# Kernel tuning notes

Hardware: AMD Instinct MI355X
Metric: run time of the kernel (lower is better)

## Reference

```python
import jax, jax.numpy as jnp
import numpy as np

B, S, D, H, P = 4, 2048, 1024, 16, 10
DK = D // H

def setup_inputs() -> dict:
    key = jax.random.key(0)
    ks = jax.random.split(key, 12)
    inp = {
        'q': jax.random.normal(ks[0], (B, S, D), jnp.float32),
        'k': jax.random.normal(ks[1], (B, S, D), jnp.float32),
        'v': jax.random.normal(ks[2], (B, S, D), jnp.float32),
        # causal mask, broadcastable over batch/heads
        'mask': jnp.tril(jnp.ones((S, S), jnp.int32))[None, None, :, :],
        'Wq': jax.random.normal(ks[3], (D, D), jnp.float32) * (1.0 / np.sqrt(D)),
        'bq': jnp.zeros((D,), jnp.float32),
        'Wk': jax.random.normal(ks[4], (D, D), jnp.float32) * (1.0 / np.sqrt(D)),
        'bk': jnp.zeros((D,), jnp.float32),
        'Wv': jax.random.normal(ks[5], (D, D), jnp.float32) * (1.0 / np.sqrt(D)),
        'bv': jnp.zeros((D,), jnp.float32),
        'Wo': jax.random.normal(ks[6], (D, D), jnp.float32) * (1.0 / np.sqrt(D)),
        'bo': jnp.zeros((D,), jnp.float32),
        'prefix_k': jax.random.normal(ks[7], (H, P, DK), jnp.float32) * 0.02,
        'prefix_v': jax.random.normal(ks[8], (H, P, DK), jnp.float32) * 0.02,
    }
    return inp

def reference(q, k, v, mask, Wq, bq, Wk, bk, Wv, bv, Wo, bo, prefix_k, prefix_v):
    bs, sq, d = q.shape
    h, p, dk = prefix_k.shape
    # projections -> [B, H, S, dk]
    Q = (q @ Wq + bq).reshape(bs, sq, h, dk).transpose(0, 2, 1, 3)
    K = (k @ Wk + bk).reshape(bs, -1, h, dk).transpose(0, 2, 1, 3)
    V = (v @ Wv + bv).reshape(bs, -1, h, dk).transpose(0, 2, 1, 3)
    # prepend learnable prefix K/V along the key axis
    pK = jnp.broadcast_to(prefix_k[None], (bs, h, p, dk))
    pV = jnp.broadcast_to(prefix_v[None], (bs, h, p, dk))
    K = jnp.concatenate([pK, K], axis=2)  # [B,H,P+S,dk]
    V = jnp.concatenate([pV, V], axis=2)
    # extend mask: prefix positions always visible
    pref_mask = jnp.ones(mask.shape[:3] + (p,), mask.dtype)
    full_mask = jnp.concatenate([pref_mask, mask], axis=-1)  # [.,.,S,P+S]
    scores = jnp.einsum('bhqd,bhkd->bhqk', Q, K) / np.sqrt(dk).astype(jnp.float32)
    scores = jnp.where(full_mask == 0, jnp.asarray(-1e9, scores.dtype), scores)
    attn = jax.nn.softmax(scores, axis=-1)  # dropout in eval mode: identity
    out = jnp.einsum('bhqk,bhkd->bhqd', attn, V)
    out = out.transpose(0, 2, 1, 3).reshape(bs, sq, d)
    return out @ Wo + bo
```

## Files before the change

### kernel.cpp

```cpp
#include <hip/hip_runtime.h>

typedef __bf16 bf16x8 __attribute__((ext_vector_type(8)));
typedef __bf16 bf16x4 __attribute__((ext_vector_type(4)));
typedef float f32x4 __attribute__((ext_vector_type(4)));

constexpr int Sq = 2048, Dd = 1024, Hn = 16, Pn = 10, DK = 64;
constexpr int SKPAD = 2112;
constexpr int NBH = 64;
constexpr float LOG2E = 1.44269504088896340736f;

__device__ __forceinline__ float exp2_fast(float x) {
  return __builtin_amdgcn_exp2f(x);
}

__device__ __forceinline__ unsigned short f2bf(float f) {
  unsigned int u = __float_as_uint(f);
  u += 0x7fffu + ((u >> 16) & 1u);
  return (unsigned short)(u >> 16);
}

__device__ __forceinline__ void gload_lds16(const void* g, void* l) {
  __builtin_amdgcn_global_load_lds(
      (const __attribute__((address_space(1))) void*)g,
      (__attribute__((address_space(3))) void*)l, 16, 0, 0);
}

__device__ __forceinline__ f32x4 mfma16(bf16x8 a, bf16x8 b, f32x4 c) {
  return __builtin_amdgcn_mfma_f32_16x16x32_bf16(a, b, c, 0, 0, 0);
}

__global__ void k_cvt3(const float* __restrict__ i0, const float* __restrict__ i1,
                       const float* __restrict__ i2, unsigned short* __restrict__ o0,
                       unsigned short* __restrict__ o1, unsigned short* __restrict__ o2,
                       int n4) {
  const float* in; unsigned short* out;
  switch (blockIdx.y) {
    case 0: in = i0; out = o0; break;
    case 1: in = i1; out = o1; break;
    default: in = i2; out = o2; break;
  }
  int i = blockIdx.x * blockDim.x + threadIdx.x;
  int st = gridDim.x * blockDim.x;
  for (; i < n4; i += st) {
    float4 v = reinterpret_cast<const float4*>(in)[i];
    ushort4 r;
    r.x = f2bf(v.x); r.y = f2bf(v.y); r.z = f2bf(v.z); r.w = f2bf(v.w);
    reinterpret_cast<ushort4*>(out)[i] = r;
  }
}

__global__ void k_wt(const float* __restrict__ W0, const float* __restrict__ W1,
                     const float* __restrict__ W2, const float* __restrict__ W3,
                     unsigned short* __restrict__ T0, unsigned short* __restrict__ T1,
                     unsigned short* __restrict__ T2, unsigned short* __restrict__ T3) {
  __shared__ float tile[32][33];
  const float* W; unsigned short* T;
  switch (blockIdx.z) {
    case 0: W = W0; T = T0; break;
    case 1: W = W1; T = T1; break;
    case 2: W = W2; T = T2; break;
    default: W = W3; T = T3; break;
  }
  int n0 = blockIdx.x * 32, k0 = blockIdx.y * 32;
  int tx = threadIdx.x, ty = threadIdx.y;
  for (int r = ty; r < 32; r += 8)
    tile[r][tx] = W[(size_t)(k0 + r) * Dd + n0 + tx];
  __syncthreads();
  for (int r = ty; r < 32; r += 8)
    T[(size_t)(n0 + r) * Dd + k0 + tx] = f2bf(tile[tx][r]);
}

__global__ void k_fill(const float* __restrict__ pk, const float* __restrict__ pv,
                       unsigned short* __restrict__ Kb, unsigned short* __restrict__ Vt) {
  int bh = blockIdx.x;
  int h = bh & (Hn - 1);
  unsigned short* Kbh = Kb + (size_t)bh * SKPAD * DK;
  unsigned short* Vth = Vt + (size_t)bh * DK * SKPAD;
  for (int i = threadIdx.x; i < Pn * DK; i += blockDim.x) {
    int p = i >> 6, dk = i & 63;
    float kv = pk[((size_t)h * Pn + p) * DK + dk];
    float vv = pv[((size_t)h * Pn + p) * DK + dk];
    Kbh[p * DK + dk] = f2bf(kv);
    Vth[dk * SKPAD + p] = f2bf(vv);
  }
  constexpr int ZR = SKPAD - (Pn + Sq);
  for (int i = threadIdx.x; i < ZR * DK; i += blockDim.x) {
    int r = i >> 6, c = i & 63;
    Kbh[(Pn + Sq + r) * DK + c] = 0;
    Vth[c * SKPAD + (Pn + Sq + r)] = 0;
  }
}

__device__ __forceinline__ void gemm_body(
    const unsigned short* __restrict__ A, const unsigned short* __restrict__ Bt,
    const float* __restrict__ bias, unsigned short* __restrict__ outB,
    float* __restrict__ outF, int mode, float scale,
    unsigned short* As, unsigned short* Bs) {
  int tid = threadIdx.x;
  int w = tid >> 6, l = tid & 63;
  int lq = l & 15, lg = l >> 4;
  int bx = blockIdx.x;
  int tm = bx >> 3, tn = bx & 7;
  int brow = tm * 128, bcol = tn * 128;
  int wm = w >> 1, wn = w & 1;

  f32x4 acc[4][4];
#pragma unroll
  for (int m = 0; m < 4; ++m)
#pragma unroll
    for (int n = 0; n < 4; ++n) acc[m][n] = (f32x4){0.f, 0.f, 0.f, 0.f};

  for (int kt = 0; kt < 1024; kt += 64) {
#pragma unroll
    for (int it = 0; it < 4; ++it) {
      int c = it * 256 + tid;
      int row = c >> 3, col = c & 7;
      gload_lds16(A + (size_t)(brow + row) * 1024 + kt + col * 8,
                  As + (size_t)(it * 256 + w * 64) * 8);
      gload_lds16(Bt + (size_t)(bcol + row) * 1024 + kt + col * 8,
                  Bs + (size_t)(it * 256 + w * 64) * 8);
    }
    asm volatile("s_waitcnt vmcnt(0)" ::: "memory");
    __syncthreads();
    const bf16x8* As8 = reinterpret_cast<const bf16x8*>(As);
    const bf16x8* Bs8 = reinterpret_cast<const bf16x8*>(Bs);
#pragma unroll
    for (int ks = 0; ks < 2; ++ks) {
      bf16x8 af[4], bfv[4];
#pragma unroll
      for (int m = 0; m < 4; ++m)
        af[m] = As8[(size_t)(wm * 64 + m * 16 + lq) * 8 + ks * 4 + lg];
#pragma unroll
      for (int n = 0; n < 4; ++n)
        bfv[n] = Bs8[(size_t)(wn * 64 + n * 16 + lq) * 8 + ks * 4 + lg];
#pragma unroll
      for (int m = 0; m < 4; ++m)
#pragma unroll
        for (int n = 0; n < 4; ++n)
          acc[m][n] = mfma16(af[m], bfv[n], acc[m][n]);
    }
    __syncthreads();
  }

#pragma unroll
  for (int n = 0; n < 4; ++n) {
    int N = bcol + wn * 64 + n * 16 + lq;
    float bv = bias[N];
#pragma unroll
    for (int m = 0; m < 4; ++m) {
      int M0 = brow + wm * 64 + m * 16 + lg * 4;
#pragma unroll
      for (int r = 0; r < 4; ++r) {
        float val = (acc[m][n][r] + bv) * scale;
        int Mr = M0 + r;
        if (mode == 3) {
          outF[(size_t)Mr * 1024 + N] = val;
        } else {
          int b = Mr >> 11, s = Mr & 2047;
          int h = N >> 6, dk = N & 63;
          size_t idx;
          if (mode == 0)      idx = (((size_t)(b * Hn + h)) * Sq + s) * DK + dk;
          else if (mode == 1) idx = (((size_t)(b * Hn + h)) * SKPAD + Pn + s) * DK + dk;
          else                idx = (((size_t)(b * Hn + h)) * DK + dk) * SKPAD + Pn + s;
          outB[idx] = f2bf(val);
        }
      }
    }
  }
}

__global__ __launch_bounds__(256, 4) void k_gemm_qkv(
    const unsigned short* __restrict__ Aq, const unsigned short* __restrict__ Ak,
    const unsigned short* __restrict__ Av,
    const unsigned short* __restrict__ Wq, const unsigned short* __restrict__ Wk,
    const unsigned short* __restrict__ Wv,
    const float* __restrict__ bq, const float* __restrict__ bk,
    const float* __restrict__ bv,
    unsigned short* __restrict__ Qo, unsigned short* __restrict__ Ko,
    unsigned short* __restrict__ Vo, float qscale) {
  __shared__ unsigned short As[128 * 64];
  __shared__ unsigned short Bs[128 * 64];
  const unsigned short *A, *Bt; const float* bias; unsigned short* outB;
  int mode; float scale;
  switch (blockIdx.y) {
    case 0:  A = Aq; Bt = Wq; bias = bq; outB = Qo; mode = 0; scale = qscale; break;
    case 1:  A = Ak; Bt = Wk; bias = bk; outB = Ko; mode = 1; scale = 1.f; break;
    default: A = Av; Bt = Wv; bias = bv; outB = Vo; mode = 2; scale = 1.f; break;
  }
  gemm_body(A, Bt, bias, outB, nullptr, mode, scale, As, Bs);
}

__global__ __launch_bounds__(256, 4) void k_gemm_o(
    const unsigned short* __restrict__ A, const unsigned short* __restrict__ Bt,
    const float* __restrict__ bias, float* __restrict__ outF) {
  __shared__ unsigned short As[128 * 64];
  __shared__ unsigned short Bs[128 * 64];
  gemm_body(A, Bt, bias, nullptr, outF, 3, 1.0f, As, Bs);
}

__global__ __launch_bounds__(256, 4) void k_attn(
    const unsigned short* __restrict__ Qb, const unsigned short* __restrict__ Kb,
    const unsigned short* __restrict__ Vt, unsigned short* __restrict__ O) {
  __shared__ unsigned short Ks[2][64 * 64];
  __shared__ unsigned short Vs[2][64 * 64];
  __shared__ unsigned short Ps[4][16 * 64];
  int tid = threadIdx.x;
  int w = tid >> 6, l = tid & 63;
  int lq = l & 15, lg = l >> 4;
  int bh = blockIdx.x;
  int pi = blockIdx.y;
  int qtL = pi, qtH = 31 - pi;
  int nktL = qtL + 2;
  int nktH = qtH + 2;
  int qsA[2] = {qtL * 64, qtH * 64};

  bf16x8 qf[2][2];
#pragma unroll
  for (int qt = 0; qt < 2; ++qt) {
    const unsigned short* Qg = Qb + ((size_t)bh * Sq + qsA[qt] + w * 16) * DK;
#pragma unroll
    for (int ks = 0; ks < 2; ++ks)
      qf[qt][ks] = *reinterpret_cast<const bf16x8*>(
          Qg + (size_t)lq * DK + ks * 32 + lg * 8);
  }

  const unsigned short* Kg = Kb + (size_t)bh * SKPAD * DK;
  const unsigned short* Vg = Vt + (size_t)bh * DK * SKPAD;

  float m_run[2] = {-1e30f, -1e30f};
  float l_part[2] = {0.f, 0.f};
  f32x4 oacc[2][4];
#pragma unroll
  for (int qt = 0; qt < 2; ++qt)
#pragma unroll
    for (int n = 0; n < 4; ++n) oacc[qt][n] = (f32x4){0.f, 0.f, 0.f, 0.f};

  unsigned short* Pw = &Ps[w][0];

  auto STAGE = [&](int b, int t) {
    int kt = t * 64;
#pragma unroll
    for (int it = 0; it < 2; ++it) {
      int dst = (it * 256 + tid) * 16;
      int srcK = dst ^ (((dst >> 7) & 7) << 4);
      gload_lds16((const char*)(Kg + (size_t)kt * DK) + srcK,
                  (char*)Ks[b] + (size_t)(it * 256 + w * 64) * 16);
    }
#pragma unroll
    for (int it = 0; it < 2; ++it) {
      int dst = (it * 256 + tid) * 16;
      int row = dst >> 7;
      int colb = (dst & 127) ^ ((row & 7) << 4);
      gload_lds16((const char*)(Vg + (size_t)row * SKPAD + kt) + colb,
                  (char*)Vs[b] + (size_t)(it * 256 + w * 64) * 16);
    }
  };

  STAGE(0, 0);
  asm volatile("s_waitcnt vmcnt(0)" ::: "memory");
  __syncthreads();

  for (int t = 0; t < nktH; ++t) {
    int bsel = t & 1;
    if (t + 1 < nktH) STAGE(bsel ^ 1, t + 1);
    int kt = t * 64;

#pragma unroll
    for (int qt = 0; qt < 2; ++qt) {
      if (qt == 0 && t >= nktL) continue;
      int qs = qsA[qt];
      if (kt > qs + w * 16 + 15 + Pn) continue;

      f32x4 st[4];
#pragma unroll
      for (int m = 0; m < 4; ++m) st[m] = (f32x4){0.f, 0.f, 0.f, 0.f};
      __builtin_amdgcn_s_setprio(1);
#pragma unroll
      for (int ks = 0; ks < 2; ++ks) {
#pragma unroll
        for (int m = 0; m < 4; ++m) {
          int krow = m * 16 + lq;
          int byt = (krow * 128 + ks * 64 + lg * 16) ^ ((krow & 7) << 4);
          bf16x8 kf = *reinterpret_cast<const bf16x8*>((const char*)Ks[bsel] + byt);
          st[m] = mfma16(kf, qf[qt][ks], st[m]);
        }
      }
      __builtin_amdgcn_s_setprio(0);

      if (kt + 63 > qs + w * 16 + Pn) {
        int qrowP = qs + w * 16 + lq + Pn;
#pragma unroll
        for (int m = 0; m < 4; ++m)
#pragma unroll
          for (int r = 0; r < 4; ++r) {
            int key = kt + m * 16 + lg * 4 + r;
            st[m][r] = (key <= qrowP) ? st[m][r] : -1e30f;
          }
      }

      float mx = fmaxf(fmaxf(st[0][0], st[0][1]), fmaxf(st[0][2], st[0][3]));
#pragma unroll
      for (int m = 1; m < 4; ++m)
        mx = fmaxf(mx, fmaxf(fmaxf(st[m][0], st[m][1]), fmaxf(st[m][2], st[m][3])));
      if (__any(mx > m_run[qt] + 8.f)) {
        float gmx = fmaxf(mx, __shfl_xor(mx, 16));
        gmx = fmaxf(gmx, __shfl_xor(gmx, 32));
        float mnew = fmaxf(m_run[qt], gmx);
        float alpha = exp2_fast(m_run[qt] - mnew);
        m_run[qt] = mnew;
        l_part[qt] *= alpha;
        float ar[4];
#pragma unroll
        for (int r = 0; r < 4; ++r) ar[r] = __shfl(alpha, lg * 4 + r);
#pragma unroll
        for (int n = 0; n < 4; ++n)
#pragma unroll
          for (int r = 0; r < 4; ++r) oacc[qt][n][r] *= ar[r];
      }
      float rs = 0.f;
#pragma unroll
      for (int m = 0; m < 4; ++m) {
        bf16x4 p4;
#pragma unroll
        for (int r = 0; r < 4; ++r) {
          float p = exp2_fast(st[m][r] - m_run[qt]);
          rs += p;
          p4[r] = (__bf16)p;
        }
        int byt = (lq * 128 + m * 32 + lg * 8) ^ ((lq & 7) << 4);
        *reinterpret_cast<bf16x4*>((char*)Pw + byt) = p4;
      }
      l_part[qt] += rs;

      __builtin_amdgcn_s_setprio(1);
#pragma unroll
      for (int ks = 0; ks < 2; ++ks) {
        int pbyt = (lq * 128 + ks * 64 + lg * 16) ^ ((lq & 7) << 4);
        bf16x8 pf = *reinterpret_cast<const bf16x8*>((const char*)Pw + pbyt);
#pragma unroll
        for (int n = 0; n < 4; ++n) {
          int dv = n * 16 + lq;
          int vbyt = (dv * 128 + ks * 64 + lg * 16) ^ ((dv & 7) << 4);
          bf16x8 vf = *reinterpret_cast<const bf16x8*>((const char*)Vs[bsel] + vbyt);
          oacc[qt][n] = mfma16(pf, vf, oacc[qt][n]);
        }
      }
      __builtin_amdgcn_s_setprio(0);
    }
    asm volatile("s_waitcnt vmcnt(0)" ::: "memory");
    __syncthreads();
  }

  int b = bh >> 4, h = bh & 15;
#pragma unroll
  for (int qt = 0; qt < 2; ++qt) {
    float ls = l_part[qt];
    ls += __shfl_xor(ls, 16);
    ls += __shfl_xor(ls, 32);
    float lr[4];
#pragma unroll
    for (int r = 0; r < 4; ++r) lr[r] = 1.0f / __shfl(ls, lg * 4 + r);
#pragma unroll
    for (int n = 0; n < 4; ++n)
#pragma unroll
      for (int r = 0; r < 4; ++r) {
        int qrow2 = qsA[qt] + w * 16 + lg * 4 + r;
        size_t idx = ((size_t)b * Sq + qrow2) * Dd + h * DK + n * 16 + lq;
        O[idx] = f2bf(oacc[qt][n][r] * lr[r]);
      }
  }
}

extern "C" void kernel_launch(void* const* d_in, const int* in_sizes, int n_in,
                              void* d_out, int out_size, void* d_ws, size_t ws_size,
                              hipStream_t stream) {
  (void)in_sizes; (void)n_in; (void)out_size; (void)ws_size;
  const float* q  = (const float*)d_in[0];
  const float* k  = (const float*)d_in[1];
  const float* v  = (const float*)d_in[2];
  const float* Wq = (const float*)d_in[4];
  const float* bq = (const float*)d_in[5];
  const float* Wk = (const float*)d_in[6];
  const float* bk = (const float*)d_in[7];
  const float* Wv = (const float*)d_in[8];
  const float* bv = (const float*)d_in[9];
  const float* Wo = (const float*)d_in[10];
  const float* bo = (const float*)d_in[11];
  const float* pk = (const float*)d_in[12];
  const float* pv = (const float*)d_in[13];

  unsigned short* wsp = (unsigned short*)d_ws;
  size_t off = 0;
  auto take = [&](size_t elems) { unsigned short* p = wsp + off; off += elems; return p; };
  unsigned short* qc  = take(8388608);
  unsigned short* kc  = take(8388608);
  unsigned short* vc  = take(8388608);
  unsigned short* wqt = take(1048576);
  unsigned short* wkt = take(1048576);
  unsigned short* wvt = take(1048576);
  unsigned short* wot = take(1048576);
  unsigned short* Qbf = take(8388608);
  unsigned short* KbB = take((size_t)NBH * SKPAD * DK);
  unsigned short* VtB = take((size_t)NBH * DK * SKPAD);
  unsigned short* Ob  = qc;
  float* outF = (float*)d_out;

  k_cvt3<<<dim3(1024, 3), 256, 0, stream>>>(q, k, v, qc, kc, vc, 8388608 / 4);
  k_wt<<<dim3(32, 32, 4), dim3(32, 8), 0, stream>>>(Wq, Wk, Wv, Wo, wqt, wkt, wvt, wot);
  k_fill<<<64, 256, 0, stream>>>(pk, pv, KbB, VtB);
  k_gemm_qkv<<<dim3(512, 3), 256, 0, stream>>>(qc, kc, vc, wqt, wkt, wvt,
                                               bq, bk, bv, Qbf, KbB, VtB,
                                               0.125f * LOG2E);
  k_attn<<<dim3(NBH, 16), 256, 0, stream>>>(Qbf, KbB, VtB, Ob);
  k_gemm_o<<<512, 256, 0, stream>>>(Ob, wot, bo, outF);
}
```

Before: 222.5 us.

## Fuse fp32-to-bf16 input conversion into QKV GEMM and remap block order

Removes the separate k_cvt3 kernel that converted q/k/v to bf16. The QKV GEMM now reads fp32 activations directly, converts them in registers and writes bf16 tiles to LDS, so the intermediate bf16 arrays are never written and re-read. Both GEMMs also get a flat 1D grid with a remapped block index, which changes which tiles run together and may improve L2 reuse of weights. The cost is that each activation tile is reloaded and reconverted once per N-tile (8 times), and the A loads become synchronous register loads instead of async global-to-LDS copies.

```diff
diff --git a/kernel.cpp b/kernel.cpp
--- a/kernel.cpp
+++ b/kernel.cpp
@@ -27,26 +27,6 @@
 
 __device__ __forceinline__ f32x4 mfma16(bf16x8 a, bf16x8 b, f32x4 c) {
   return __builtin_amdgcn_mfma_f32_16x16x32_bf16(a, b, c, 0, 0, 0);
-}
-
-__global__ void k_cvt3(const float* __restrict__ i0, const float* __restrict__ i1,
-                       const float* __restrict__ i2, unsigned short* __restrict__ o0,
-                       unsigned short* __restrict__ o1, unsigned short* __restrict__ o2,
-                       int n4) {
-  const float* in; unsigned short* out;
-  switch (blockIdx.y) {
-    case 0: in = i0; out = o0; break;
-    case 1: in = i1; out = o1; break;
-    default: in = i2; out = o2; break;
-  }
-  int i = blockIdx.x * blockDim.x + threadIdx.x;
-  int st = gridDim.x * blockDim.x;
-  for (; i < n4; i += st) {
-    float4 v = reinterpret_cast<const float4*>(in)[i];
-    ushort4 r;
-    r.x = f2bf(v.x); r.y = f2bf(v.y); r.z = f2bf(v.z); r.w = f2bf(v.w);
-    reinterpret_cast<ushort4*>(out)[i] = r;
-  }
 }
 
 __global__ void k_wt(const float* __restrict__ W0, const float* __restrict__ W1,
@@ -91,87 +71,9 @@
   }
 }
 
-__device__ __forceinline__ void gemm_body(
-    const unsigned short* __restrict__ A, const unsigned short* __restrict__ Bt,
-    const float* __restrict__ bias, unsigned short* __restrict__ outB,
-    float* __restrict__ outF, int mode, float scale,
-    unsigned short* As, unsigned short* Bs) {
-  int tid = threadIdx.x;
-  int w = tid >> 6, l = tid & 63;
-  int lq = l & 15, lg = l >> 4;
-  int bx = blockIdx.x;
-  int tm = bx >> 3, tn = bx & 7;
-  int brow = tm * 128, bcol = tn * 128;
-  int wm = w >> 1, wn = w & 1;
-
-  f32x4 acc[4][4];
-#pragma unroll
-  for (int m = 0; m < 4; ++m)
-#pragma unroll
-    for (int n = 0; n < 4; ++n) acc[m][n] = (f32x4){0.f, 0.f, 0.f, 0.f};
-
-  for (int kt = 0; kt < 1024; kt += 64) {
-#pragma unroll
-    for (int it = 0; it < 4; ++it) {
-      int c = it * 256 + tid;
-      int row = c >> 3, col = c & 7;
-      gload_lds16(A + (size_t)(brow + row) * 1024 + kt + col * 8,
-                  As + (size_t)(it * 256 + w * 64) * 8);
-      gload_lds16(Bt + (size_t)(bcol + row) * 1024 + kt + col * 8,
-                  Bs + (size_t)(it * 256 + w * 64) * 8);
-    }
-    asm volatile("s_waitcnt vmcnt(0)" ::: "memory");
-    __syncthreads();
-    const bf16x8* As8 = reinterpret_cast<const bf16x8*>(As);
-    const bf16x8* Bs8 = reinterpret_cast<const bf16x8*>(Bs);
-#pragma unroll
-    for (int ks = 0; ks < 2; ++ks) {
-      bf16x8 af[4], bfv[4];
-#pragma unroll
-      for (int m = 0; m < 4; ++m)
-        af[m] = As8[(size_t)(wm * 64 + m * 16 + lq) * 8 + ks * 4 + lg];
-#pragma unroll
-      for (int n = 0; n < 4; ++n)
-        bfv[n] = Bs8[(size_t)(wn * 64 + n * 16 + lq) * 8 + ks * 4 + lg];
-#pragma unroll
-      for (int m = 0; m < 4; ++m)
-#pragma unroll
-        for (int n = 0; n < 4; ++n)
-          acc[m][n] = mfma16(af[m], bfv[n], acc[m][n]);
-    }
-    __syncthreads();
-  }
-
-#pragma unroll
-  for (int n = 0; n < 4; ++n) {
-    int N = bcol + wn * 64 + n * 16 + lq;
-    float bv = bias[N];
-#pragma unroll
-    for (int m = 0; m < 4; ++m) {
-      int M0 = brow + wm * 64 + m * 16 + lg * 4;
-#pragma unroll
-      for (int r = 0; r < 4; ++r) {
-        float val = (acc[m][n][r] + bv) * scale;
-        int Mr = M0 + r;
-        if (mode == 3) {
-          outF[(size_t)Mr * 1024 + N] = val;
-        } else {
-          int b = Mr >> 11, s = Mr & 2047;
-          int h = N >> 6, dk = N & 63;
-          size_t idx;
-          if (mode == 0)      idx = (((size_t)(b * Hn + h)) * Sq + s) * DK + dk;
-          else if (mode == 1) idx = (((size_t)(b * Hn + h)) * SKPAD + Pn + s) * DK + dk;
-          else                idx = (((size_t)(b * Hn + h)) * DK + dk) * SKPAD + Pn + s;
-          outB[idx] = f2bf(val);
-        }
-      }
-    }
-  }
-}
-
 __global__ __launch_bounds__(256, 4) void k_gemm_qkv(
-    const unsigned short* __restrict__ Aq, const unsigned short* __restrict__ Ak,
-    const unsigned short* __restrict__ Av,
+    const float* __restrict__ Aq, const float* __restrict__ Ak,
+    const float* __restrict__ Av,
     const unsigned short* __restrict__ Wq, const unsigned short* __restrict__ Wk,
     const unsigned short* __restrict__ Wv,
     const float* __restrict__ bq, const float* __restrict__ bk,
@@ -180,14 +82,101 @@
     unsigned short* __restrict__ Vo, float qscale) {
   __shared__ unsigned short As[128 * 64];
   __shared__ unsigned short Bs[128 * 64];
-  const unsigned short *A, *Bt; const float* bias; unsigned short* outB;
-  int mode; float scale;
-  switch (blockIdx.y) {
-    case 0:  A = Aq; Bt = Wq; bias = bq; outB = Qo; mode = 0; scale = qscale; break;
-    case 1:  A = Ak; Bt = Wk; bias = bk; outB = Ko; mode = 1; scale = 1.f; break;
-    default: A = Av; Bt = Wv; bias = bv; outB = Vo; mode = 2; scale = 1.f; break;
-  }
-  gemm_body(A, Bt, bias, outB, nullptr, mode, scale, As, Bs);
+  int bx0 = blockIdx.x;
+  int orig = (bx0 & 7) * 192 + (bx0 >> 3);
+  int stream = orig >> 9, within = orig & 511;
+
+  const float* A32; const unsigned short* Bt; const float* bias;
+  unsigned short* outB; float scale;
+  switch (stream) {
+    case 0:  A32 = Aq; Bt = Wq; bias = bq; outB = Qo; scale = qscale; break;
+    case 1:  A32 = Ak; Bt = Wk; bias = bk; outB = Ko; scale = 1.f; break;
+    default: A32 = Av; Bt = Wv; bias = bv; outB = Vo; scale = 1.f; break;
+  }
+
+  int tid = threadIdx.x;
+  int w = tid >> 6, l = tid & 63;
+  int lq = l & 15, lg = l >> 4;
+  int tm = within >> 3, tn = within & 7;
+  int brow = tm * 128, bcol = tn * 128;
+  int wm = w >> 1, wn = w & 1;
+
+  f32x4 acc[4][4];
+#pragma unroll
+  for (int m = 0; m < 4; ++m)
+#pragma unroll
+    for (int n = 0; n < 4; ++n) acc[m][n] = (f32x4){0.f, 0.f, 0.f, 0.f};
+
+  int arow = tid >> 3, acol = tid & 7;
+
+  for (int kt = 0; kt < 1024; kt += 64) {
+#pragma unroll
+    for (int it = 0; it < 4; ++it) {
+      int c = it * 256 + tid;
+      int row = c >> 3, col = c & 7;
+      gload_lds16(Bt + (size_t)(bcol + row) * 1024 + kt + col * 8,
+                  Bs + (size_t)(it * 256 + w * 64) * 8);
+    }
+    float4 a0[4], a1[4];
+#pragma unroll
+    for (int it = 0; it < 4; ++it) {
+      const float* src = A32 + (size_t)(brow + it * 32 + arow) * 1024 + kt + acol * 8;
+      a0[it] = *reinterpret_cast<const float4*>(src);
+      a1[it] = *reinterpret_cast<const float4*>(src + 4);
+    }
+#pragma unroll
+    for (int it = 0; it < 4; ++it) {
+      ushort4 lo, hi;
+      lo.x = f2bf(a0[it].x); lo.y = f2bf(a0[it].y);
+      lo.z = f2bf(a0[it].z); lo.w = f2bf(a0[it].w);
+      hi.x = f2bf(a1[it].x); hi.y = f2bf(a1[it].y);
+      hi.z = f2bf(a1[it].z); hi.w = f2bf(a1[it].w);
+      ushort4* dst = reinterpret_cast<ushort4*>(As + (size_t)(it * 256 + tid) * 8);
+      dst[0] = lo; dst[1] = hi;
+    }
+    asm volatile("s_waitcnt vmcnt(0)" ::: "memory");
+    __syncthreads();
+    const bf16x8* As8 = reinterpret_cast<const bf16x8*>(As);
+    const bf16x8* Bs8 = reinterpret_cast<const bf16x8*>(Bs);
+#pragma unroll
+    for (int ks = 0; ks < 2; ++ks) {
+      bf16x8 af[4], bfv[4];
+#pragma unroll
+      for (int m = 0; m < 4; ++m)
+        af[m] = As8[(size_t)(wm * 64 + m * 16 + lq) * 8 + ks * 4 + lg];
+#pragma unroll
+      for (int n = 0; n < 4; ++n)
+        bfv[n] = Bs8[(size_t)(wn * 64 + n * 16 + lq) * 8 + ks * 4 + lg];
+#pragma unroll
+      for (int m = 0; m < 4; ++m)
+#pragma unroll
+        for (int n = 0; n < 4; ++n)
+          acc[m][n] = mfma16(af[m], bfv[n], acc[m][n]);
+    }
+    __syncthreads();
+  }
+
+#pragma unroll
+  for (int n = 0; n < 4; ++n) {
+    int N = bcol + wn * 64 + n * 16 + lq;
+    float bv = bias[N];
+#pragma unroll
+    for (int m = 0; m < 4; ++m) {
+      int M0 = brow + wm * 64 + m * 16 + lg * 4;
+#pragma unroll
+      for (int r = 0; r < 4; ++r) {
+        float val = (acc[m][n][r] + bv) * scale;
+        int Mr = M0 + r;
+        int b = Mr >> 11, s = Mr & 2047;
+        int h = N >> 6, dk = N & 63;
+        size_t idx;
+        if (stream == 0)      idx = (((size_t)(b * Hn + h)) * Sq + s) * DK + dk;
+        else if (stream == 1) idx = (((size_t)(b * Hn + h)) * SKPAD + Pn + s) * DK + dk;
+        else                  idx = (((size_t)(b * Hn + h)) * DK + dk) * SKPAD + Pn + s;
+        outB[idx] = f2bf(val);
+      }
+    }
+  }
 }
 
 __global__ __launch_bounds__(256, 4) void k_gemm_o(
@@ -195,7 +184,65 @@
     const float* __restrict__ bias, float* __restrict__ outF) {
   __shared__ unsigned short As[128 * 64];
   __shared__ unsigned short Bs[128 * 64];
-  gemm_body(A, Bt, bias, nullptr, outF, 3, 1.0f, As, Bs);
+  int bx0 = blockIdx.x;
+  int within = (bx0 & 7) * 64 + (bx0 >> 3);
+  int tid = threadIdx.x;
+  int w = tid >> 6, l = tid & 63;
+  int lq = l & 15, lg = l >> 4;
+  int tm = within >> 3, tn = within & 7;
+  int brow = tm * 128, bcol = tn * 128;
+  int wm = w >> 1, wn = w & 1;
+
+  f32x4 acc[4][4];
+#pragma unroll
+  for (int m = 0; m < 4; ++m)
+#pragma unroll
+    for (int n = 0; n < 4; ++n) acc[m][n] = (f32x4){0.f, 0.f, 0.f, 0.f};
+
+  for (int kt = 0; kt < 1024; kt += 64) {
+#pragma unroll
+    for (int it = 0; it < 4; ++it) {
+      int c = it * 256 + tid;
+      int row = c >> 3, col = c & 7;
+      gload_lds16(A + (size_t)(brow + row) * 1024 + kt + col * 8,
+                  As + (size_t)(it * 256 + w * 64) * 8);
+      gload_lds16(Bt + (size_t)(bcol + row) * 1024 + kt + col * 8,
+                  Bs + (size_t)(it * 256 + w * 64) * 8);
+    }
+    asm volatile("s_waitcnt vmcnt(0)" ::: "memory");
+    __syncthreads();
+    const bf16x8* As8 = reinterpret_cast<const bf16x8*>(As);
+    const bf16x8* Bs8 = reinterpret_cast<const bf16x8*>(Bs);
+#pragma unroll
+    for (int ks = 0; ks < 2; ++ks) {
+      bf16x8 af[4], bfv[4];
+#pragma unroll
+      for (int m = 0; m < 4; ++m)
+        af[m] = As8[(size_t)(wm * 64 + m * 16 + lq) * 8 + ks * 4 + lg];
+#pragma unroll
+      for (int n = 0; n < 4; ++n)
+        bfv[n] = Bs8[(size_t)(wn * 64 + n * 16 + lq) * 8 + ks * 4 + lg];
+#pragma unroll
+      for (int m = 0; m < 4; ++m)
+#pragma unroll
+        for (int n = 0; n < 4; ++n)
+          acc[m][n] = mfma16(af[m], bfv[n], acc[m][n]);
+    }
+    __syncthreads();
+  }
+
+#pragma unroll
+  for (int n = 0; n < 4; ++n) {
+    int N = bcol + wn * 64 + n * 16 + lq;
+    float bv = bias[N];
+#pragma unroll
+    for (int m = 0; m < 4; ++m) {
+      int M0 = brow + wm * 64 + m * 16 + lg * 4;
+#pragma unroll
+      for (int r = 0; r < 4; ++r)
+        outF[(size_t)(M0 + r) * 1024 + N] = acc[m][n][r] + bv;
+    }
+  }
 }
 
 __global__ __launch_bounds__(256, 4) void k_attn(
@@ -392,9 +439,7 @@
   unsigned short* wsp = (unsigned short*)d_ws;
   size_t off = 0;
   auto take = [&](size_t elems) { unsigned short* p = wsp + off; off += elems; return p; };
-  unsigned short* qc  = take(8388608);
-  unsigned short* kc  = take(8388608);
-  unsigned short* vc  = take(8388608);
+  unsigned short* Ob  = take(8388608);
   unsigned short* wqt = take(1048576);
   unsigned short* wkt = take(1048576);
   unsigned short* wvt = take(1048576);
@@ -402,15 +447,13 @@
   unsigned short* Qbf = take(8388608);
   unsigned short* KbB = take((size_t)NBH * SKPAD * DK);
   unsigned short* VtB = take((size_t)NBH * DK * SKPAD);
-  unsigned short* Ob  = qc;
   float* outF = (float*)d_out;
 
-  k_cvt3<<<dim3(1024, 3), 256, 0, stream>>>(q, k, v, qc, kc, vc, 8388608 / 4);
   k_wt<<<dim3(32, 32, 4), dim3(32, 8), 0, stream>>>(Wq, Wk, Wv, Wo, wqt, wkt, wvt, wot);
   k_fill<<<64, 256, 0, stream>>>(pk, pv, KbB, VtB);
-  k_gemm_qkv<<<dim3(512, 3), 256, 0, stream>>>(qc, kc, vc, wqt, wkt, wvt,
-                                               bq, bk, bv, Qbf, KbB, VtB,
-                                               0.125f * LOG2E);
+  k_gemm_qkv<<<1536, 256, 0, stream>>>(q, k, v, wqt, wkt, wvt,
+                                       bq, bk, bv, Qbf, KbB, VtB,
+                                       0.125f * LOG2E);
   k_attn<<<dim3(NBH, 16), 256, 0, stream>>>(Qbf, KbB, VtB, Ob);
   k_gemm_o<<<512, 256, 0, stream>>>(Ob, wot, bo, outF);
 }
```

New measurement: 254.0 us. 14.2% more time.
